# Kernel optimization log

Measured on AMD Instinct MI355X. Metric: run time of the kernel, lower is better.

The kernel has to match this reference:

```python
import jax, jax.numpy as jnp
import numpy as np

N_LAYER, N_HEAD, N_EMBD, D_STATE, VOCAB, N_POS = 12, 12, 768, 128, 60, 1024
ID_ID = 0


def _ln(x, g, b):
    m = x.mean(-1, keepdims=True)
    v = ((x - m) ** 2).mean(-1, keepdims=True)
    return (x - m) / jnp.sqrt(v + 1e-5) * g + b


def _prefix_states(input_ids, mul):
    # POST states: s_0 = id ; s_{t+1} = mul[x_t, s_t] ; states[:, t] = s_{t+1}
    B = input_ids.shape[0]

    def step(s, x_t):
        s2 = mul[x_t, s]
        return s2, s2

    s0 = jnp.full((B,), ID_ID, dtype=input_ids.dtype)
    _, post = jax.lax.scan(step, s0, input_ids.T)  # [T, B]
    return post.T  # [B, T]


def _forward(input_ids, mul, tok_emb, state_emb, state_proj_w, state_proj_b, wpe,
             ln1_g, ln1_b, attn_w, attn_b, attn_proj_w, attn_proj_b,
             ln2_g, ln2_b, fc_w, fc_b, mlp_proj_w, mlp_proj_b,
             lnf_g, lnf_b, head_w, head_b):
    B, T = input_ids.shape
    post = _prefix_states(input_ids, mul)
    # pre_state[t] = s_{t-1}; pre_state[0] = id  (inject_mode='clean')
    pre = jnp.concatenate([jnp.full((B, 1), ID_ID, dtype=post.dtype), post[:, :-1]], axis=1)
    # clean + input_add: mask == 1 at every position, fusion hook inactive
    s = state_emb[pre] @ state_proj_w + state_proj_b  # [B, T, E]
    h = tok_emb[input_ids] + s + wpe[:T]              # GPT-2 adds wpe to inputs_embeds
    causal = jnp.tril(jnp.ones((T, T), dtype=bool))
    scale = 1.0 / np.sqrt(N_EMBD // N_HEAD)
    for l in range(N_LAYER):
        a = _ln(h, ln1_g[l], ln1_b[l])
        q, k, v = jnp.split(a @ attn_w[l] + attn_b[l], 3, axis=-1)
        q = q.reshape(B, T, N_HEAD, -1)
        k = k.reshape(B, T, N_HEAD, -1)
        v = v.reshape(B, T, N_HEAD, -1)
        scores = jnp.einsum('bthd,bshd->bhts', q, k) * scale
        scores = jnp.where(causal, scores, jnp.float32(-1e9))
        p = jax.nn.softmax(scores, axis=-1)
        o = jnp.einsum('bhts,bshd->bthd', p, v).reshape(B, T, N_EMBD)
        h = h + o @ attn_proj_w[l] + attn_proj_b[l]
        m = _ln(h, ln2_g[l], ln2_b[l])
        h = h + jax.nn.gelu(m @ fc_w[l] + fc_b[l], approximate=True) @ mlp_proj_w[l] + mlp_proj_b[l]
    h = _ln(h, lnf_g, lnf_b)
    return h @ head_w + head_b  # logits [B, T, VOCAB]


def setup_inputs():
    key = jax.random.key(0)
    ks = jax.random.split(key, 16)
    B, T = 8, 512
    E, L, DS, V = N_EMBD, N_LAYER, D_STATE, VOCAB
    n = lambda k, shp: jax.random.normal(k, shp, dtype=jnp.float32) * 0.02
    return {
        "input_ids": jax.random.randint(ks[0], (B, T), 0, V),
        "mul": jax.random.randint(ks[1], (V, V), 0, V),
        "tok_emb": n(ks[2], (V, E)),
        "state_emb": n(ks[3], (V, DS)),
        "state_proj_w": n(ks[4], (DS, E)),
        "state_proj_b": jnp.zeros((E,), jnp.float32),
        "wpe": n(ks[5], (N_POS, E)),
        "ln1_g": jnp.ones((L, E), jnp.float32),
        "ln1_b": jnp.zeros((L, E), jnp.float32),
        "attn_w": n(ks[6], (L, E, 3 * E)),
        "attn_b": jnp.zeros((L, 3 * E), jnp.float32),
        "attn_proj_w": n(ks[7], (L, E, E)),
        "attn_proj_b": jnp.zeros((L, E), jnp.float32),
        "ln2_g": jnp.ones((L, E), jnp.float32),
        "ln2_b": jnp.zeros((L, E), jnp.float32),
        "fc_w": n(ks[8], (L, E, 4 * E)),
        "fc_b": jnp.zeros((L, 4 * E), jnp.float32),
        "mlp_proj_w": n(ks[9], (L, 4 * E, E)),
        "mlp_proj_b": jnp.zeros((L, E), jnp.float32),
        "lnf_g": jnp.ones((E,), jnp.float32),
        "lnf_b": jnp.zeros((E,), jnp.float32),
        "head_w": n(ks[10], (E, V)),
        "head_b": jnp.zeros((V,), jnp.float32),
    }


def reference(input_ids, mul, tok_emb, state_emb, state_proj_w, state_proj_b, wpe,
              ln1_g, ln1_b, attn_w, attn_b, attn_proj_w, attn_proj_b,
              ln2_g, ln2_b, fc_w, fc_b, mlp_proj_w, mlp_proj_b,
              lnf_g, lnf_b, head_w, head_b):
    return _forward(input_ids, mul, tok_emb, state_emb, state_proj_w, state_proj_b, wpe,
                    ln1_g, ln1_b, attn_w, attn_b, attn_proj_w, attn_proj_b,
                    ln2_g, ln2_b, fc_w, fc_b, mlp_proj_w, mlp_proj_b,
                    lnf_g, lnf_b, head_w, head_b)
```

## Files before the change

kernel.cpp:

```cpp
#include <hip/hip_runtime.h>
#include <cmath>

using bf16 = __bf16;
typedef __bf16 bf16x8 __attribute__((ext_vector_type(8)));
typedef float f32x4 __attribute__((ext_vector_type(4)));

#define N_LAYER 12
#define EMB 768
#define E3 2304
#define FF 3072
#define SEQ 512
#define NB 8
#define BT 4096
#define NH 12
#define HD 64
#define VOC 60
#define DST 128

__device__ __forceinline__ void gll16(const bf16* g, bf16* l) {
    __builtin_amdgcn_global_load_lds(
        (const __attribute__((address_space(1))) void*)g,
        (__attribute__((address_space(3))) void*)l,
        16, 0, 0);
}

__global__ __launch_bounds__(1024)
void scan_kernel(const int* __restrict__ ids, const int* __restrict__ mul, int* __restrict__ pre)
{
    __shared__ int smul[VOC * VOC];
    __shared__ int sx[SEQ];
    __shared__ int chunk_end[16 * VOC];
    __shared__ int entry[17];
    int b = blockIdx.x;
    int tid = threadIdx.x;
    for (int i = tid; i < VOC * VOC; i += 1024) smul[i] = mul[i];
    for (int i = tid; i < SEQ; i += 1024) sx[i] = ids[b * SEQ + i];
    __syncthreads();
    if (tid < 16 * VOC) {
        int c = tid / VOC, s0 = tid % VOC;
        int s = s0;
        int base = c * 32;
        for (int j = 0; j < 32; j++) s = smul[sx[base + j] * VOC + s];
        chunk_end[c * VOC + s0] = s;
    }
    __syncthreads();
    if (tid == 0) {
        int s = 0;
        entry[0] = 0;
        for (int c = 0; c < 16; c++) { s = chunk_end[c * VOC + s]; entry[c + 1] = s; }
    }
    __syncthreads();
    if (tid < 16) {
        int c = tid;
        int s = entry[c];
        for (int j = 0; j < 32; j++) {
            int t = c * 32 + j;
            pre[b * SEQ + t] = s;
            s = smul[sx[t] * VOC + s];
        }
    }
}

__global__ __launch_bounds__(256)
void pst_kernel(const float* __restrict__ se, const float* __restrict__ w,
                const float* __restrict__ bias, float* __restrict__ pst)
{
    int v = blockIdx.x;
    int e = blockIdx.y * 256 + threadIdx.x;
    float acc = bias[e];
    for (int k = 0; k < DST; k++) acc += se[v * DST + k] * w[k * EMB + e];
    pst[v * EMB + e] = acc;
}

__device__ __forceinline__ void ln_stats(float& s, float& s2, float* ps, int tid)
{
    for (int o = 32; o > 0; o >>= 1) { s += __shfl_xor(s, o, 64); s2 += __shfl_xor(s2, o, 64); }
    int wave = tid >> 6, lane = tid & 63;
    if (lane == 0) { ps[wave] = s; ps[4 + wave] = s2; }
    __syncthreads();
    s = ps[0] + ps[1] + ps[2] + ps[3];
    s2 = ps[4] + ps[5] + ps[6] + ps[7];
}

__global__ __launch_bounds__(256)
void embed_ln_kernel(const int* __restrict__ ids, const int* __restrict__ pre,
                     const float* __restrict__ tok_emb, const float* __restrict__ pst,
                     const float* __restrict__ wpe,
                     const float* __restrict__ g, const float* __restrict__ b,
                     float* __restrict__ h, bf16* __restrict__ y)
{
    int t = blockIdx.x;
    int pos = t & (SEQ - 1);
    int id = ids[t], pr = pre[t];
    int tid = threadIdx.x;
    float vals[3];
    float s = 0.f, s2 = 0.f;
    for (int j = 0; j < 3; j++) {
        int e = tid + j * 256;
        float xv = tok_emb[id * EMB + e] + pst[pr * EMB + e] + wpe[pos * EMB + e];
        h[(size_t)t * EMB + e] = xv;
        vals[j] = xv; s += xv; s2 += xv * xv;
    }
    __shared__ float ps[8];
    ln_stats(s, s2, ps, tid);
    float m = s * (1.0f / EMB);
    float var = s2 * (1.0f / EMB) - m * m;
    float inv = rsqrtf(var + 1e-5f);
    for (int j = 0; j < 3; j++) {
        int e = tid + j * 256;
        y[(size_t)t * EMB + e] = (bf16)((vals[j] - m) * inv * g[e] + b[e]);
    }
}

template<int S>
__global__ __launch_bounds__(256)
void reduce_ln_kernel(const float* __restrict__ p, const float* __restrict__ bias,
                      float* __restrict__ h,
                      const float* __restrict__ g, const float* __restrict__ b,
                      bf16* __restrict__ y)
{
    int t = blockIdx.x;
    int tid = threadIdx.x;
    float vals[3];
    float s = 0.f, s2 = 0.f;
    for (int j = 0; j < 3; j++) {
        int e = tid + j * 256;
        size_t i = (size_t)t * EMB + e;
        float acc = bias[e] + h[i];
        for (int sp = 0; sp < S; sp++) acc += p[(size_t)sp * ((size_t)BT * EMB) + i];
        h[i] = acc;
        vals[j] = acc; s += acc; s2 += acc * acc;
    }
    __shared__ float ps[8];
    ln_stats(s, s2, ps, tid);
    float m = s * (1.0f / EMB);
    float var = s2 * (1.0f / EMB) - m * m;
    float inv = rsqrtf(var + 1e-5f);
    for (int j = 0; j < 3; j++) {
        int e = tid + j * 256;
        y[(size_t)t * EMB + e] = (bf16)((vals[j] - m) * inv * g[e] + b[e]);
    }
}

__global__ __launch_bounds__(256)
void convw_kernel(const float* __restrict__ W, bf16* __restrict__ WT, int K, int N)
{
    __shared__ float tile[32][33];
    int kb = blockIdx.y * 32, nb = blockIdx.x * 32;
    const float* Wl = W + (size_t)blockIdx.z * K * N;
    bf16* WTl = WT + (size_t)blockIdx.z * K * N;
    int tx = threadIdx.x & 31, ty = threadIdx.x >> 5;
    for (int i = ty; i < 32; i += 8) {
        int k = kb + i, n = nb + tx;
        if (k < K && n < N) tile[i][tx] = Wl[(size_t)k * N + n];
    }
    __syncthreads();
    for (int i = ty; i < 32; i += 8) {
        int n = nb + i, k = kb + tx;
        if (k < K && n < N) WTl[(size_t)n * K + k] = (bf16)tile[tx][i];
    }
}

__global__ __launch_bounds__(256)
void vtrans_kernel(const bf16* __restrict__ qkv, bf16* __restrict__ vT)
{
    int bh = blockIdx.y;
    int b = bh / NH, hh = bh - b * NH;
    int idx = blockIdx.x * 256 + threadIdx.x;
    int d = idx >> 9, t = idx & 511;
    vT[((size_t)bh * HD + d) * SEQ + t] = qkv[((size_t)(b * SEQ + t)) * E3 + 2 * EMB + hh * HD + d];
}

__global__ __launch_bounds__(256)
void fattn_kernel(const bf16* __restrict__ qkv, const bf16* __restrict__ vT, bf16* __restrict__ Og)
{
    __shared__ bf16 sK[128 * 64];
    __shared__ bf16 sV[64 * 128];
    __shared__ bf16 sP[4][16 * 128];
    int mq = blockIdx.x;
    int bh = blockIdx.y;
    int b = bh / NH, hh = bh - b * NH;
    int tid = threadIdx.x, lane = tid & 63, wave = tid >> 6;
    int r = lane & 15, q = lane >> 4;

    const bf16* Qg = qkv + (size_t)(b * SEQ + mq * 64) * E3 + hh * HD;
    const bf16* Kg = qkv + (size_t)(b * SEQ) * E3 + EMB + hh * HD;
    const bf16* Vg = vT + (size_t)bh * HD * SEQ;

    bf16x8 af[2];
    {
        const bf16* qrow = Qg + (size_t)(wave * 16 + r) * E3 + q * 8;
        af[0] = *(const bf16x8*)(qrow);
        af[1] = *(const bf16x8*)(qrow + 32);
    }

    float mrun[4], lrun[4];
    f32x4 acco[4];
    for (int e = 0; e < 4; e++) { mrun[e] = -1e30f; lrun[e] = 0.f; }
    for (int no = 0; no < 4; no++)
        for (int e = 0; e < 4; e++) acco[no][e] = 0.f;

    int KT = mq / 2 + 1;
    bf16* sPw = sP[wave];

    for (int kt = 0; kt < KT; kt++) {
        {
            int row = tid >> 3;
            int cb = (tid & 7) * 8;
            for (int rd = 0; rd < 4; rd++) {
                int rr = rd * 32 + row;
                bf16x8 kv = *(const bf16x8*)(Kg + (size_t)(kt * 128 + rr) * E3 + cb);
                *(bf16x8*)(sK + ((rr * 64 + cb) ^ ((rr & 7) << 3))) = kv;
            }
            int rowv = tid >> 4;
            int cbv = (tid & 15) * 8;
            for (int rd = 0; rd < 4; rd++) {
                int rr = rd * 16 + rowv;
                bf16x8 vv = *(const bf16x8*)(Vg + (size_t)rr * SEQ + kt * 128 + cbv);
                *(bf16x8*)(sV + ((rr * 128 + cbv) ^ ((rr & 7) << 3))) = vv;
            }
        }
        __syncthreads();

        f32x4 acc[8];
        for (int ni = 0; ni < 8; ni++)
            for (int e = 0; e < 4; e++) acc[ni][e] = 0.f;
        for (int ks = 0; ks < 2; ks++) {
            for (int ni = 0; ni < 8; ni++) {
                int row = ni * 16 + r;
                bf16x8 bk = *(const bf16x8*)(sK + ((row * 64 + ks * 32 + q * 8) ^ ((row & 7) << 3)));
                acc[ni] = __builtin_amdgcn_mfma_f32_16x16x32_bf16(af[ks], bk, acc[ni], 0, 0, 0);
            }
        }

        bool dm = (kt * 128 + 127) > (mq * 64);
        for (int ni = 0; ni < 8; ni++) {
            int col = kt * 128 + ni * 16 + r;
            for (int e = 0; e < 4; e++) {
                float s = acc[ni][e] * 0.125f;
                if (dm) {
                    int rowg = mq * 64 + wave * 16 + q * 4 + e;
                    if (col > rowg) s = -1e30f;
                }
                acc[ni][e] = s;
            }
        }

        float corr[4];
        for (int e = 0; e < 4; e++) {
            float mx = -1e30f;
            for (int ni = 0; ni < 8; ni++) mx = fmaxf(mx, acc[ni][e]);
            for (int o2 = 1; o2 < 16; o2 <<= 1) mx = fmaxf(mx, __shfl_xor(mx, o2, 64));
            float mn = fmaxf(mrun[e], mx);
            corr[e] = __expf(mrun[e] - mn);
            mrun[e] = mn;
            float ps = 0.f;
            for (int ni = 0; ni < 8; ni++) {
                float p = __expf(acc[ni][e] - mn);
                acc[ni][e] = p;
                ps += p;
            }
            for (int o2 = 1; o2 < 16; o2 <<= 1) ps += __shfl_xor(ps, o2, 64);
            lrun[e] = lrun[e] * corr[e] + ps;
        }
        for (int no = 0; no < 4; no++)
            for (int e = 0; e < 4; e++) acco[no][e] *= corr[e];

        for (int ni = 0; ni < 8; ni++) {
            for (int e = 0; e < 4; e++) {
                int prow = q * 4 + e;
                sPw[(prow * 128 + ni * 16 + r) ^ ((prow & 7) << 3)] = (bf16)acc[ni][e];
            }
        }
        for (int ks2 = 0; ks2 < 4; ks2++) {
            bf16x8 pa = *(const bf16x8*)(sPw + ((r * 128 + ks2 * 32 + q * 8) ^ ((r & 7) << 3)));
            for (int no = 0; no < 4; no++) {
                int row = no * 16 + r;
                bf16x8 bv = *(const bf16x8*)(sV + ((row * 128 + ks2 * 32 + q * 8) ^ ((row & 7) << 3)));
                acco[no] = __builtin_amdgcn_mfma_f32_16x16x32_bf16(pa, bv, acco[no], 0, 0, 0);
            }
        }
        __syncthreads();
    }

    bf16* orow = Og + (size_t)(b * SEQ + mq * 64 + wave * 16) * EMB + hh * HD;
    for (int e = 0; e < 4; e++) {
        float inv = 1.0f / lrun[e];
        for (int no = 0; no < 4; no++)
            orow[(size_t)(q * 4 + e) * EMB + no * 16 + r] = (bf16)(acco[no][e] * inv);
    }
}

__global__ __launch_bounds__(256)
void reduce_head_kernel(const float* __restrict__ p, const float* __restrict__ bias,
                        float* __restrict__ out)
{
    int i = blockIdx.x * 256 + threadIdx.x;
    int c = i % VOC;
    float acc = bias[c];
    for (int s = 0; s < 8; s++) acc += p[(size_t)s * ((size_t)BT * VOC) + i];
    out[i] = acc;
}

template<int MODE, int KSPLIT = 1>
__global__ __launch_bounds__(256)
void gemm_bt(const bf16* __restrict__ Ag, const bf16* __restrict__ Bg,
             const float* __restrict__ bias, bf16* __restrict__ Cb, float* __restrict__ Cf,
             int M, int N, int K, int lda, int ldb, int ldc,
             long long sAb, long long sAh, long long sBb, long long sBh,
             long long sCb, long long sCh)
{
    __shared__ union { bf16 ab[2][128 * 32]; float st[4][16 * 64]; } sm;
    int z = blockIdx.z, zs = 0;
    if constexpr (KSPLIT > 1) { zs = z % KSPLIT; z /= KSPLIT; }
    int zb = z / NH, zh = z - zb * NH;
    Ag += zb * sAb + zh * sAh;
    Bg += zb * sBb + zh * sBh;
    long long coff = zb * sCb + zh * sCh;

    if constexpr (MODE == 6 || MODE == 7) Cf += (size_t)zs * M * ldc;

    int m0 = blockIdx.y * 128, n0 = blockIdx.x * 128;
    int tid = threadIdx.x, lane = tid & 63, wave = tid >> 6;
    int wm = (wave >> 1) * 64, wn = (wave & 1) * 64;
    int r = lane & 15, q = lane >> 4;

    f32x4 acc[4][4];
    for (int mi = 0; mi < 4; mi++)
        for (int ni = 0; ni < 4; ni++)
            for (int e = 0; e < 4; e++) acc[mi][ni][e] = 0.f;

    bf16* la = sm.ab[0];
    bf16* lb = sm.ab[1];
    int srow = wave * 16 + (lane >> 2);
    int scol = (lane & 3) * 8;
    const bf16* pA = Ag + (size_t)(m0 + srow) * lda + scol;
    const bf16* pB = Bg + (size_t)(n0 + srow) * ldb + scol;
    bf16* lA0 = la + (wave * 16) * 32;
    bf16* lA1 = la + (wave * 16 + 64) * 32;
    bf16* lB0 = lb + (wave * 16) * 32;
    bf16* lB1 = lb + (wave * 16 + 64) * 32;
    size_t stepA = (size_t)64 * lda, stepB = (size_t)64 * ldb;

    int kbeg = 0, kend = K;
    if constexpr (KSPLIT > 1) { int Kc = K / KSPLIT; kbeg = zs * Kc; kend = kbeg + Kc; }

    for (int k0 = kbeg; k0 < kend; k0 += 32) {
        gll16(pA + k0, lA0);
        gll16(pA + k0 + stepA, lA1);
        gll16(pB + k0, lB0);
        gll16(pB + k0 + stepB, lB1);
        __syncthreads();
        bf16x8 af[4], bq[4];
        for (int mi = 0; mi < 4; mi++) af[mi] = *(const bf16x8*)(la + (wm + mi * 16 + r) * 32 + q * 8);
        for (int ni = 0; ni < 4; ni++) bq[ni] = *(const bf16x8*)(lb + (wn + ni * 16 + r) * 32 + q * 8);
        for (int mi = 0; mi < 4; mi++)
            for (int ni = 0; ni < 4; ni++)
                acc[mi][ni] = __builtin_amdgcn_mfma_f32_16x16x32_bf16(af[mi], bq[ni], acc[mi][ni], 0, 0, 0);
        __syncthreads();
    }

    if constexpr (MODE == 7) {
        for (int mi = 0; mi < 4; mi++) {
            for (int ni = 0; ni < 4; ni++) {
                int colg = n0 + wn + ni * 16 + r;
                if (colg >= N) continue;
                for (int e = 0; e < 4; e++) {
                    int rowg = m0 + wm + mi * 16 + q * 4 + e;
                    if (rowg >= M) continue;
                    Cf[(size_t)coff + (size_t)rowg * ldc + colg] = acc[mi][ni][e];
                }
            }
        }
        return;
    }

    const float* biasp = (MODE == 6) ? nullptr : bias;

    float* st = sm.st[wave];
    bool wvalid = (n0 + wn) < N;
    for (int mi = 0; mi < 4; mi++) {
        if (wvalid) {
            for (int ni = 0; ni < 4; ni++)
                for (int e = 0; e < 4; e++)
                    st[(q * 4 + e) * 64 + ni * 16 + r] = acc[mi][ni][e];
        }
        asm volatile("s_waitcnt lgkmcnt(0)" ::: "memory");
        if (wvalid) {
            for (int it = 0; it < 2; it++) {
                int task = lane + it * 64;
                int row = task >> 3, cc = (task & 7) * 8;
                f32x4 v0 = *(const f32x4*)(st + row * 64 + cc);
                f32x4 v1 = *(const f32x4*)(st + row * 64 + cc + 4);
                int colg = n0 + wn + cc;
                int rowg = m0 + wm + mi * 16 + row;
                if (biasp) {
                    f32x4 b0 = *(const f32x4*)(biasp + colg);
                    f32x4 b1 = *(const f32x4*)(biasp + colg + 4);
                    v0 += b0; v1 += b1;
                }
                size_t off = (size_t)coff + (size_t)rowg * ldc + colg;
                if constexpr (MODE == 0) {
                    bf16x8 pk;
                    for (int j = 0; j < 4; j++) { pk[j] = (bf16)v0[j]; pk[4 + j] = (bf16)v1[j]; }
                    *(bf16x8*)(Cb + off) = pk;
                } else if constexpr (MODE == 1) {
                    float w[8];
                    for (int j = 0; j < 4; j++) { w[j] = v0[j]; w[4 + j] = v1[j]; }
                    bf16x8 pk;
                    for (int j = 0; j < 8; j++) {
                        float x = w[j];
                        float gx = 0.5f * x * (1.0f + tanhf(0.7978845608028654f * (x + 0.044715f * x * x * x)));
                        pk[j] = (bf16)gx;
                    }
                    *(bf16x8*)(Cb + off) = pk;
                } else {
                    *(f32x4*)(Cf + off) = v0;
                    *(f32x4*)(Cf + off + 4) = v1;
                }
            }
        }
        asm volatile("s_waitcnt lgkmcnt(0)" ::: "memory");
    }
}

extern "C" void kernel_launch(void* const* d_in, const int* in_sizes, int n_in,
                              void* d_out, int out_size, void* d_ws, size_t ws_size,
                              hipStream_t stream)
{
    (void)in_sizes; (void)n_in; (void)out_size; (void)ws_size;
    const int*   input_ids    = (const int*)d_in[0];
    const int*   mul          = (const int*)d_in[1];
    const float* tok_emb      = (const float*)d_in[2];
    const float* state_emb    = (const float*)d_in[3];
    const float* state_proj_w = (const float*)d_in[4];
    const float* state_proj_b = (const float*)d_in[5];
    const float* wpe          = (const float*)d_in[6];
    const float* ln1_g        = (const float*)d_in[7];
    const float* ln1_b        = (const float*)d_in[8];
    const float* attn_w       = (const float*)d_in[9];
    const float* attn_b       = (const float*)d_in[10];
    const float* attn_proj_w  = (const float*)d_in[11];
    const float* attn_proj_b  = (const float*)d_in[12];
    const float* ln2_g        = (const float*)d_in[13];
    const float* ln2_b        = (const float*)d_in[14];
    const float* fc_w         = (const float*)d_in[15];
    const float* fc_b         = (const float*)d_in[16];
    const float* mlp_proj_w   = (const float*)d_in[17];
    const float* mlp_proj_b   = (const float*)d_in[18];
    const float* lnf_g        = (const float*)d_in[19];
    const float* lnf_b        = (const float*)d_in[20];
    const float* head_w       = (const float*)d_in[21];
    const float* head_b       = (const float*)d_in[22];
    float* out = (float*)d_out;

    char* ws = (char*)d_ws;
    size_t off = 0;
    auto alloc = [&](size_t bytes) -> char* {
        char* p = ws + off;
        off += (bytes + 255) & ~(size_t)255;
        return p;
    };
    bf16*  wT_attn = (bf16*)alloc((size_t)N_LAYER * E3 * EMB * 2);
    bf16*  wT_ap   = (bf16*)alloc((size_t)N_LAYER * EMB * EMB * 2);
    bf16*  wT_fc   = (bf16*)alloc((size_t)N_LAYER * FF * EMB * 2);
    bf16*  wT_mp   = (bf16*)alloc((size_t)N_LAYER * EMB * FF * 2);
    bf16*  wT_head = (bf16*)alloc((size_t)VOC * EMB * 2);
    float* pst     = (float*)alloc((size_t)VOC * EMB * 4);
    int*   pre     = (int*)alloc((size_t)BT * 4);
    float* h       = (float*)alloc((size_t)BT * EMB * 4);
    bf16*  xb      = (bf16*)alloc((size_t)BT * EMB * 2);
    bf16*  qkv     = (bf16*)alloc((size_t)BT * E3 * 2);
    bf16*  vT      = (bf16*)alloc((size_t)NB * NH * HD * SEQ * 2);
    bf16*  o       = (bf16*)alloc((size_t)BT * EMB * 2);
    bf16*  fcout   = (bf16*)alloc((size_t)BT * FF * 2);
    float* pbuf    = (float*)alloc((size_t)4 * BT * EMB * 4);

    convw_kernel<<<dim3(E3 / 32, EMB / 32, N_LAYER), 256, 0, stream>>>(attn_w, wT_attn, EMB, E3);
    convw_kernel<<<dim3(EMB / 32, EMB / 32, N_LAYER), 256, 0, stream>>>(attn_proj_w, wT_ap, EMB, EMB);
    convw_kernel<<<dim3(FF / 32, EMB / 32, N_LAYER), 256, 0, stream>>>(fc_w, wT_fc, EMB, FF);
    convw_kernel<<<dim3(EMB / 32, FF / 32, N_LAYER), 256, 0, stream>>>(mlp_proj_w, wT_mp, FF, EMB);
    convw_kernel<<<dim3(2, EMB / 32, 1), 256, 0, stream>>>(head_w, wT_head, EMB, VOC);

    scan_kernel<<<NB, 1024, 0, stream>>>(input_ids, mul, pre);
    pst_kernel<<<dim3(VOC, 3), 256, 0, stream>>>(state_emb, state_proj_w, state_proj_b, pst);
    embed_ln_kernel<<<BT, 256, 0, stream>>>(input_ids, pre, tok_emb, pst, wpe,
                                            ln1_g, ln1_b, h, xb);

    for (int l = 0; l < N_LAYER; l++) {
        gemm_bt<0><<<dim3(E3 / 128, BT / 128, 1), 256, 0, stream>>>(
            xb, wT_attn + (size_t)l * E3 * EMB, attn_b + l * E3, qkv, nullptr,
            BT, E3, EMB, EMB, EMB, E3, 0, 0, 0, 0, 0, 0);
        vtrans_kernel<<<dim3(128, NB * NH), 256, 0, stream>>>(qkv, vT);
        fattn_kernel<<<dim3(SEQ / 64, NB * NH), 256, 0, stream>>>(qkv, vT, o);
        gemm_bt<6, 4><<<dim3(EMB / 128, BT / 128, 4), 256, 0, stream>>>(
            o, wT_ap + (size_t)l * EMB * EMB, nullptr, nullptr, pbuf,
            BT, EMB, EMB, EMB, EMB, EMB, 0, 0, 0, 0, 0, 0);
        reduce_ln_kernel<4><<<BT, 256, 0, stream>>>(
            pbuf, attn_proj_b + l * EMB, h, ln2_g + l * EMB, ln2_b + l * EMB, xb);
        gemm_bt<1><<<dim3(FF / 128, BT / 128, 1), 256, 0, stream>>>(
            xb, wT_fc + (size_t)l * FF * EMB, fc_b + l * FF, fcout, nullptr,
            BT, FF, EMB, EMB, EMB, FF, 0, 0, 0, 0, 0, 0);
        gemm_bt<6, 4><<<dim3(EMB / 128, BT / 128, 4), 256, 0, stream>>>(
            fcout, wT_mp + (size_t)l * EMB * FF, nullptr, nullptr, pbuf,
            BT, EMB, FF, FF, FF, EMB, 0, 0, 0, 0, 0, 0);
        const float* ng = (l < N_LAYER - 1) ? (ln1_g + (l + 1) * EMB) : lnf_g;
        const float* nb2 = (l < N_LAYER - 1) ? (ln1_b + (l + 1) * EMB) : lnf_b;
        reduce_ln_kernel<4><<<BT, 256, 0, stream>>>(
            pbuf, mlp_proj_b + l * EMB, h, ng, nb2, xb);
    }
    gemm_bt<7, 8><<<dim3(1, BT / 128, 8), 256, 0, stream>>>(
        xb, wT_head, nullptr, nullptr, pbuf,
        BT, VOC, EMB, EMB, EMB, VOC, 0, 0, 0, 0, 0, 0);
    reduce_head_kernel<<<(BT * VOC) / 256, 256, 0, stream>>>(pbuf, head_b, out);
}
```

Measured before the change: 2.902 ms.

## Add 256x256 triple-buffered 8-wave GEMM for all transformer layer projections

Introduces a new gemm8 kernel with 512 threads, 256x256 output tiles and a three-stage LDS ring fed by global_load_lds. Each k-step is split into two halves, so loads for the step two ahead overlap the MFMA work, with setprio raised around the MFMA bursts. It replaces the 128x128 double-sync gemm_bt for the QKV, attention projection, FC and MLP projection GEMMs, and trims gemm_bt down to the head-only path. The larger tiles cut A/B refetch and barrier overhead, at the cost of fewer blocks: for example, the split-K projections launch only 3x16x4 = 192 blocks, and the larger LDS footprint limits occupancy.

```diff
diff --git a/kernel.cpp b/kernel.cpp
--- a/kernel.cpp
+++ b/kernel.cpp
@@ -303,22 +303,165 @@
 }
 
 template<int MODE, int KSPLIT = 1>
+__global__ __launch_bounds__(512, 2)
+void gemm8(const bf16* __restrict__ Ag, const bf16* __restrict__ Bg,
+           const float* __restrict__ bias, bf16* __restrict__ Cb, float* __restrict__ Cf,
+           int N, int K, int lda, int ldb, int ldc)
+{
+    __shared__ union {
+        bf16 stage[3][2][256 * 32];
+        float st[8][16 * 64];
+    } sm;
+
+    int zs = blockIdx.z;
+    int Kc = K / KSPLIT;
+    int kbeg = zs * Kc;
+    int NT = Kc / 32;
+    if constexpr (MODE == 6) Cf += (size_t)zs * (size_t)BT * ldc;
+
+    int m0 = blockIdx.y * 256, n0 = blockIdx.x * 256;
+    int tid = threadIdx.x, lane = tid & 63, wave = tid >> 6;
+    int wm = wave >> 2, wn = wave & 3;
+    int r = lane & 15, q = lane >> 4;
+
+    f32x4 acc[8][4];
+#pragma unroll
+    for (int mi = 0; mi < 8; mi++)
+#pragma unroll
+        for (int ni = 0; ni < 4; ni++)
+#pragma unroll
+            for (int e = 0; e < 4; e++) acc[mi][ni][e] = 0.f;
+
+    int srow = lane >> 2;
+    int scol = (lane & 3) * 8;
+    const bf16* pA0 = Ag + (size_t)(m0 + (wave) * 16 + srow) * lda + scol;
+    const bf16* pA1 = Ag + (size_t)(m0 + (8 + wave) * 16 + srow) * lda + scol;
+    const bf16* pB0 = Bg + (size_t)(n0 + (wave) * 16 + srow) * ldb + scol;
+    const bf16* pB1 = Bg + (size_t)(n0 + (8 + wave) * 16 + srow) * ldb + scol;
+    int l0 = wave * 512;
+    int l1 = (8 + wave) * 512;
+
+    auto stageA = [&](int kt, int b) {
+        int k0 = kbeg + kt * 32;
+        gll16(pA0 + k0, &sm.stage[b][0][l0]);
+        gll16(pA1 + k0, &sm.stage[b][0][l1]);
+    };
+    auto stageB = [&](int kt, int b) {
+        int k0 = kbeg + kt * 32;
+        gll16(pB0 + k0, &sm.stage[b][1][l0]);
+        gll16(pB1 + k0, &sm.stage[b][1][l1]);
+    };
+
+    stageA(0, 0); stageB(0, 0);
+    stageA(1 < NT ? 1 : 0, 1); stageB(1 < NT ? 1 : 0, 1);
+    asm volatile("s_waitcnt vmcnt(4)" ::: "memory");
+    __builtin_amdgcn_s_barrier();
+    asm volatile("" ::: "memory");
+
+    for (int t = 0; t < NT; t++) {
+        int c = t % 3;
+        const bf16* la = sm.stage[c][0];
+        const bf16* lb = sm.stage[c][1];
+        int t2 = (t + 2 < NT) ? t + 2 : NT - 1;
+        int b2 = (t + 2) % 3;
+
+        bf16x8 afr[4], bfr[4];
+#pragma unroll
+        for (int i = 0; i < 4; i++)
+            afr[i] = *(const bf16x8*)(la + (wm * 128 + i * 16 + r) * 32 + q * 8);
+#pragma unroll
+        for (int ni = 0; ni < 4; ni++)
+            bfr[ni] = *(const bf16x8*)(lb + (wn * 64 + ni * 16 + r) * 32 + q * 8);
+        stageA(t2, b2);
+        asm volatile("" ::: "memory");
+        __builtin_amdgcn_s_barrier();
+        __builtin_amdgcn_s_setprio(1);
+#pragma unroll
+        for (int i = 0; i < 4; i++)
+#pragma unroll
+            for (int ni = 0; ni < 4; ni++)
+                acc[i][ni] = __builtin_amdgcn_mfma_f32_16x16x32_bf16(afr[i], bfr[ni], acc[i][ni], 0, 0, 0);
+        __builtin_amdgcn_s_setprio(0);
+        asm volatile("" ::: "memory");
+        __builtin_amdgcn_s_barrier();
+        asm volatile("" ::: "memory");
+
+#pragma unroll
+        for (int i = 0; i < 4; i++)
+            afr[i] = *(const bf16x8*)(la + (wm * 128 + (4 + i) * 16 + r) * 32 + q * 8);
+        stageB(t2, b2);
+        asm volatile("" ::: "memory");
+        __builtin_amdgcn_s_barrier();
+        __builtin_amdgcn_s_setprio(1);
+#pragma unroll
+        for (int i = 0; i < 4; i++)
+#pragma unroll
+            for (int ni = 0; ni < 4; ni++)
+                acc[4 + i][ni] = __builtin_amdgcn_mfma_f32_16x16x32_bf16(afr[i], bfr[ni], acc[4 + i][ni], 0, 0, 0);
+        __builtin_amdgcn_s_setprio(0);
+        asm volatile("s_waitcnt vmcnt(4)" ::: "memory");
+        __builtin_amdgcn_s_barrier();
+        asm volatile("" ::: "memory");
+    }
+
+    asm volatile("s_waitcnt vmcnt(0) lgkmcnt(0)" ::: "memory");
+    __builtin_amdgcn_s_barrier();
+    asm volatile("" ::: "memory");
+
+    float* st = sm.st[wave];
+#pragma unroll 1
+    for (int mi = 0; mi < 8; mi++) {
+#pragma unroll
+        for (int ni = 0; ni < 4; ni++)
+#pragma unroll
+            for (int e = 0; e < 4; e++)
+                st[(q * 4 + e) * 64 + ni * 16 + r] = acc[mi][ni][e];
+        asm volatile("s_waitcnt lgkmcnt(0)" ::: "memory");
+        for (int it = 0; it < 2; it++) {
+            int task = lane + it * 64;
+            int row = task >> 3, cc = (task & 7) * 8;
+            f32x4 v0 = *(const f32x4*)(st + row * 64 + cc);
+            f32x4 v1 = *(const f32x4*)(st + row * 64 + cc + 4);
+            int colg = n0 + wn * 64 + cc;
+            int rowg = m0 + wm * 128 + mi * 16 + row;
+            if (MODE != 6 && bias) {
+                f32x4 b0 = *(const f32x4*)(bias + colg);
+                f32x4 b1 = *(const f32x4*)(bias + colg + 4);
+                v0 += b0; v1 += b1;
+            }
+            size_t off = (size_t)rowg * ldc + colg;
+            if constexpr (MODE == 0) {
+                bf16x8 pk;
+                for (int j = 0; j < 4; j++) { pk[j] = (bf16)v0[j]; pk[4 + j] = (bf16)v1[j]; }
+                *(bf16x8*)(Cb + off) = pk;
+            } else if constexpr (MODE == 1) {
+                float w[8];
+                for (int j = 0; j < 4; j++) { w[j] = v0[j]; w[4 + j] = v1[j]; }
+                bf16x8 pk;
+                for (int j = 0; j < 8; j++) {
+                    float x = w[j];
+                    float gx = 0.5f * x * (1.0f + tanhf(0.7978845608028654f * (x + 0.044715f * x * x * x)));
+                    pk[j] = (bf16)gx;
+                }
+                *(bf16x8*)(Cb + off) = pk;
+            } else {
+                *(f32x4*)(Cf + off) = v0;
+                *(f32x4*)(Cf + off + 4) = v1;
+            }
+        }
+        asm volatile("s_waitcnt lgkmcnt(0)" ::: "memory");
+    }
+}
+
+template<int MODE, int KSPLIT = 1>
 __global__ __launch_bounds__(256)
 void gemm_bt(const bf16* __restrict__ Ag, const bf16* __restrict__ Bg,
              const float* __restrict__ bias, bf16* __restrict__ Cb, float* __restrict__ Cf,
-             int M, int N, int K, int lda, int ldb, int ldc,
-             long long sAb, long long sAh, long long sBb, long long sBh,
-             long long sCb, long long sCh)
-{
-    __shared__ union { bf16 ab[2][128 * 32]; float st[4][16 * 64]; } sm;
-    int z = blockIdx.z, zs = 0;
-    if constexpr (KSPLIT > 1) { zs = z % KSPLIT; z /= KSPLIT; }
-    int zb = z / NH, zh = z - zb * NH;
-    Ag += zb * sAb + zh * sAh;
-    Bg += zb * sBb + zh * sBh;
-    long long coff = zb * sCb + zh * sCh;
-
-    if constexpr (MODE == 6 || MODE == 7) Cf += (size_t)zs * M * ldc;
+             int M, int N, int K, int lda, int ldb, int ldc)
+{
+    __shared__ bf16 sab[2][128 * 32];
+    int zs = blockIdx.z % KSPLIT;
+    if constexpr (MODE == 7) Cf += (size_t)zs * M * ldc;
 
     int m0 = blockIdx.y * 128, n0 = blockIdx.x * 128;
     int tid = threadIdx.x, lane = tid & 63, wave = tid >> 6;
@@ -330,8 +473,8 @@
         for (int ni = 0; ni < 4; ni++)
             for (int e = 0; e < 4; e++) acc[mi][ni][e] = 0.f;
 
-    bf16* la = sm.ab[0];
-    bf16* lb = sm.ab[1];
+    bf16* la = sab[0];
+    bf16* lb = sab[1];
     int srow = wave * 16 + (lane >> 2);
     int scol = (lane & 3) * 8;
     const bf16* pA = Ag + (size_t)(m0 + srow) * lda + scol;
@@ -342,8 +485,8 @@
     bf16* lB1 = lb + (wave * 16 + 64) * 32;
     size_t stepA = (size_t)64 * lda, stepB = (size_t)64 * ldb;
 
-    int kbeg = 0, kend = K;
-    if constexpr (KSPLIT > 1) { int Kc = K / KSPLIT; kbeg = zs * Kc; kend = kbeg + Kc; }
+    int Kc = K / KSPLIT;
+    int kbeg = zs * Kc, kend = kbeg + Kc;
 
     for (int k0 = kbeg; k0 < kend; k0 += 32) {
         gll16(pA + k0, lA0);
@@ -360,67 +503,16 @@
         __syncthreads();
     }
 
-    if constexpr (MODE == 7) {
-        for (int mi = 0; mi < 4; mi++) {
-            for (int ni = 0; ni < 4; ni++) {
-                int colg = n0 + wn + ni * 16 + r;
-                if (colg >= N) continue;
-                for (int e = 0; e < 4; e++) {
-                    int rowg = m0 + wm + mi * 16 + q * 4 + e;
-                    if (rowg >= M) continue;
-                    Cf[(size_t)coff + (size_t)rowg * ldc + colg] = acc[mi][ni][e];
-                }
-            }
-        }
-        return;
-    }
-
-    const float* biasp = (MODE == 6) ? nullptr : bias;
-
-    float* st = sm.st[wave];
-    bool wvalid = (n0 + wn) < N;
     for (int mi = 0; mi < 4; mi++) {
-        if (wvalid) {
-            for (int ni = 0; ni < 4; ni++)
-                for (int e = 0; e < 4; e++)
-                    st[(q * 4 + e) * 64 + ni * 16 + r] = acc[mi][ni][e];
-        }
-        asm volatile("s_waitcnt lgkmcnt(0)" ::: "memory");
-        if (wvalid) {
-            for (int it = 0; it < 2; it++) {
-                int task = lane + it * 64;
-                int row = task >> 3, cc = (task & 7) * 8;
-                f32x4 v0 = *(const f32x4*)(st + row * 64 + cc);
-                f32x4 v1 = *(const f32x4*)(st + row * 64 + cc + 4);
-                int colg = n0 + wn + cc;
-                int rowg = m0 + wm + mi * 16 + row;
-                if (biasp) {
-                    f32x4 b0 = *(const f32x4*)(biasp + colg);
-                    f32x4 b1 = *(const f32x4*)(biasp + colg + 4);
-                    v0 += b0; v1 += b1;
-                }
-                size_t off = (size_t)coff + (size_t)rowg * ldc + colg;
-                if constexpr (MODE == 0) {
-                    bf16x8 pk;
-                    for (int j = 0; j < 4; j++) { pk[j] = (bf16)v0[j]; pk[4 + j] = (bf16)v1[j]; }
-                    *(bf16x8*)(Cb + off) = pk;
-                } else if constexpr (MODE == 1) {
-                    float w[8];
-                    for (int j = 0; j < 4; j++) { w[j] = v0[j]; w[4 + j] = v1[j]; }
-                    bf16x8 pk;
-                    for (int j = 0; j < 8; j++) {
-                        float x = w[j];
-                        float gx = 0.5f * x * (1.0f + tanhf(0.7978845608028654f * (x + 0.044715f * x * x * x)));
-                        pk[j] = (bf16)gx;
-                    }
-                    *(bf16x8*)(Cb + off) = pk;
-                } else {
-                    *(f32x4*)(Cf + off) = v0;
-                    *(f32x4*)(Cf + off + 4) = v1;
-                }
-            }
-        }
-        asm volatile("s_waitcnt lgkmcnt(0)" ::: "memory");
+        for (int ni = 0; ni < 4; ni++) {
+            int colg = n0 + wn + ni * 16 + r;
+            if (colg >= N) continue;
+            for (int e = 0; e < 4; e++) {
+                int rowg = m0 + wm + mi * 16 + q * 4 + e;
+                if (rowg >= M) continue;
+                Cf[(size_t)rowg * ldc + colg] = acc[mi][ni][e];
+            }
+        }
     }
 }
 
@@ -488,22 +580,22 @@
                                             ln1_g, ln1_b, h, xb);
 
     for (int l = 0; l < N_LAYER; l++) {
-        gemm_bt<0><<<dim3(E3 / 128, BT / 128, 1), 256, 0, stream>>>(
+        gemm8<0><<<dim3(E3 / 256, BT / 256, 1), 512, 0, stream>>>(
             xb, wT_attn + (size_t)l * E3 * EMB, attn_b + l * E3, qkv, nullptr,
-            BT, E3, EMB, EMB, EMB, E3, 0, 0, 0, 0, 0, 0);
+            E3, EMB, EMB, EMB, E3);
         vtrans_kernel<<<dim3(128, NB * NH), 256, 0, stream>>>(qkv, vT);
         fattn_kernel<<<dim3(SEQ / 64, NB * NH), 256, 0, stream>>>(qkv, vT, o);
-        gemm_bt<6, 4><<<dim3(EMB / 128, BT / 128, 4), 256, 0, stream>>>(
+        gemm8<6, 4><<<dim3(EMB / 256, BT / 256, 4), 512, 0, stream>>>(
             o, wT_ap + (size_t)l * EMB * EMB, nullptr, nullptr, pbuf,
-            BT, EMB, EMB, EMB, EMB, EMB, 0, 0, 0, 0, 0, 0);
+            EMB, EMB, EMB, EMB, EMB);
         reduce_ln_kernel<4><<<BT, 256, 0, stream>>>(
             pbuf, attn_proj_b + l * EMB, h, ln2_g + l * EMB, ln2_b + l * EMB, xb);
-        gemm_bt<1><<<dim3(FF / 128, BT / 128, 1), 256, 0, stream>>>(
+        gemm8<1><<<dim3(FF / 256, BT / 256, 1), 512, 0, stream>>>(
             xb, wT_fc + (size_t)l * FF * EMB, fc_b + l * FF, fcout, nullptr,
-            BT, FF, EMB, EMB, EMB, FF, 0, 0, 0, 0, 0, 0);
-        gemm_bt<6, 4><<<dim3(EMB / 128, BT / 128, 4), 256, 0, stream>>>(
+            FF, EMB, EMB, EMB, FF);
+        gemm8<6, 4><<<dim3(EMB / 256, BT / 256, 4), 512, 0, stream>>>(
             fcout, wT_mp + (size_t)l * EMB * FF, nullptr, nullptr, pbuf,
-            BT, EMB, FF, FF, FF, EMB, 0, 0, 0, 0, 0, 0);
+            EMB, FF, FF, FF, EMB);
         const float* ng = (l < N_LAYER - 1) ? (ln1_g + (l + 1) * EMB) : lnf_g;
         const float* nb2 = (l < N_LAYER - 1) ? (ln1_b + (l + 1) * EMB) : lnf_b;
         reduce_ln_kernel<4><<<BT, 256, 0, stream>>>(
@@ -511,6 +603,6 @@
     }
     gemm_bt<7, 8><<<dim3(1, BT / 128, 8), 256, 0, stream>>>(
         xb, wT_head, nullptr, nullptr, pbuf,
-        BT, VOC, EMB, EMB, EMB, VOC, 0, 0, 0, 0, 0, 0);
+        BT, VOC, EMB, EMB, EMB, VOC);
     reduce_head_kernel<<<(BT * VOC) / 256, 256, 0, stream>>>(pbuf, head_b, out);
 }
```

Result: slower. 3.987 ms (+37.4%).

## Fuse V transpose into QKV GEMM epilogue and add XCD block remapping

Applied to the files above, without the earlier changes.

The QKV GEMM epilogue now also writes the V columns in transposed per-head layout, which removes the separate vtrans kernel launch and its extra read of qkv. A block-index swizzle spreads neighbouring tiles across XCDs for the GEMM and attention kernels to improve L2 locality. The epilogue staging buffer stride is padded to 68 floats to reduce LDS bank conflicts. The cost is that V is stored with strided 2-byte scalar writes, which coalesce poorly.

```diff
diff --git a/kernel.cpp b/kernel.cpp
--- a/kernel.cpp
+++ b/kernel.cpp
@@ -22,6 +22,18 @@
         (const __attribute__((address_space(1))) void*)g,
         (__attribute__((address_space(3))) void*)l,
         16, 0, 0);
+}
+
+__device__ __forceinline__ void xcd_remap(int& bx, int& by, int& bz)
+{
+    int gx = gridDim.x, gy = gridDim.y, gz = gridDim.z;
+    int nwg = gx * gy * gz;
+    int lin = (blockIdx.z * gy + blockIdx.y) * gx + blockIdx.x;
+    int swz = (lin & 7) * (nwg >> 3) + (lin >> 3);
+    bx = swz % gx;
+    int t = swz / gx;
+    by = t % gy;
+    bz = t / gy;
 }
 
 __global__ __launch_bounds__(1024)
@@ -162,23 +174,13 @@
 }
 
 __global__ __launch_bounds__(256)
-void vtrans_kernel(const bf16* __restrict__ qkv, bf16* __restrict__ vT)
-{
-    int bh = blockIdx.y;
-    int b = bh / NH, hh = bh - b * NH;
-    int idx = blockIdx.x * 256 + threadIdx.x;
-    int d = idx >> 9, t = idx & 511;
-    vT[((size_t)bh * HD + d) * SEQ + t] = qkv[((size_t)(b * SEQ + t)) * E3 + 2 * EMB + hh * HD + d];
-}
-
-__global__ __launch_bounds__(256)
 void fattn_kernel(const bf16* __restrict__ qkv, const bf16* __restrict__ vT, bf16* __restrict__ Og)
 {
     __shared__ bf16 sK[128 * 64];
     __shared__ bf16 sV[64 * 128];
     __shared__ bf16 sP[4][16 * 128];
-    int mq = blockIdx.x;
-    int bh = blockIdx.y;
+    int mq, bh, bzu;
+    xcd_remap(mq, bh, bzu);
     int b = bh / NH, hh = bh - b * NH;
     int tid = threadIdx.x, lane = tid & 63, wave = tid >> 6;
     int r = lane & 15, q = lane >> 4;
@@ -306,21 +308,16 @@
 __global__ __launch_bounds__(256)
 void gemm_bt(const bf16* __restrict__ Ag, const bf16* __restrict__ Bg,
              const float* __restrict__ bias, bf16* __restrict__ Cb, float* __restrict__ Cf,
-             int M, int N, int K, int lda, int ldb, int ldc,
-             long long sAb, long long sAh, long long sBb, long long sBh,
-             long long sCb, long long sCh)
-{
-    __shared__ union { bf16 ab[2][128 * 32]; float st[4][16 * 64]; } sm;
-    int z = blockIdx.z, zs = 0;
-    if constexpr (KSPLIT > 1) { zs = z % KSPLIT; z /= KSPLIT; }
-    int zb = z / NH, zh = z - zb * NH;
-    Ag += zb * sAb + zh * sAh;
-    Bg += zb * sBb + zh * sBh;
-    long long coff = zb * sCb + zh * sCh;
-
+             bf16* __restrict__ Vt,
+             int M, int N, int K, int lda, int ldb, int ldc)
+{
+    __shared__ union { bf16 ab[2][128 * 32]; float st[4][16 * 68]; } sm;
+    int bx, by, bz;
+    xcd_remap(bx, by, bz);
+    int zs = bz;
     if constexpr (MODE == 6 || MODE == 7) Cf += (size_t)zs * M * ldc;
 
-    int m0 = blockIdx.y * 128, n0 = blockIdx.x * 128;
+    int m0 = by * 128, n0 = bx * 128;
     int tid = threadIdx.x, lane = tid & 63, wave = tid >> 6;
     int wm = (wave >> 1) * 64, wn = (wave & 1) * 64;
     int r = lane & 15, q = lane >> 4;
@@ -342,8 +339,8 @@
     bf16* lB1 = lb + (wave * 16 + 64) * 32;
     size_t stepA = (size_t)64 * lda, stepB = (size_t)64 * ldb;
 
-    int kbeg = 0, kend = K;
-    if constexpr (KSPLIT > 1) { int Kc = K / KSPLIT; kbeg = zs * Kc; kend = kbeg + Kc; }
+    int Kc = K / KSPLIT;
+    int kbeg = zs * Kc, kend = kbeg + Kc;
 
     for (int k0 = kbeg; k0 < kend; k0 += 32) {
         gll16(pA + k0, lA0);
@@ -368,7 +365,7 @@
                 for (int e = 0; e < 4; e++) {
                     int rowg = m0 + wm + mi * 16 + q * 4 + e;
                     if (rowg >= M) continue;
-                    Cf[(size_t)coff + (size_t)rowg * ldc + colg] = acc[mi][ni][e];
+                    Cf[(size_t)rowg * ldc + colg] = acc[mi][ni][e];
                 }
             }
         }
@@ -378,46 +375,49 @@
     const float* biasp = (MODE == 6) ? nullptr : bias;
 
     float* st = sm.st[wave];
-    bool wvalid = (n0 + wn) < N;
     for (int mi = 0; mi < 4; mi++) {
-        if (wvalid) {
-            for (int ni = 0; ni < 4; ni++)
-                for (int e = 0; e < 4; e++)
-                    st[(q * 4 + e) * 64 + ni * 16 + r] = acc[mi][ni][e];
-        }
+        for (int ni = 0; ni < 4; ni++)
+            for (int e = 0; e < 4; e++)
+                st[(q * 4 + e) * 68 + ni * 16 + r] = acc[mi][ni][e];
         asm volatile("s_waitcnt lgkmcnt(0)" ::: "memory");
-        if (wvalid) {
-            for (int it = 0; it < 2; it++) {
-                int task = lane + it * 64;
-                int row = task >> 3, cc = (task & 7) * 8;
-                f32x4 v0 = *(const f32x4*)(st + row * 64 + cc);
-                f32x4 v1 = *(const f32x4*)(st + row * 64 + cc + 4);
-                int colg = n0 + wn + cc;
-                int rowg = m0 + wm + mi * 16 + row;
-                if (biasp) {
-                    f32x4 b0 = *(const f32x4*)(biasp + colg);
-                    f32x4 b1 = *(const f32x4*)(biasp + colg + 4);
-                    v0 += b0; v1 += b1;
+        for (int it = 0; it < 2; it++) {
+            int task = lane + it * 64;
+            int row = task >> 3, cc = (task & 7) * 8;
+            f32x4 v0 = *(const f32x4*)(st + row * 68 + cc);
+            f32x4 v1 = *(const f32x4*)(st + row * 68 + cc + 4);
+            int colg = n0 + wn + cc;
+            int rowg = m0 + wm + mi * 16 + row;
+            if (biasp) {
+                f32x4 b0 = *(const f32x4*)(biasp + colg);
+                f32x4 b1 = *(const f32x4*)(biasp + colg + 4);
+                v0 += b0; v1 += b1;
+            }
+            size_t off = (size_t)rowg * ldc + colg;
+            if constexpr (MODE == 8) {
+                bf16x8 pk;
+                for (int j = 0; j < 4; j++) { pk[j] = (bf16)v0[j]; pk[4 + j] = (bf16)v1[j]; }
+                *(bf16x8*)(Cb + off) = pk;
+                if (colg >= 2 * EMB) {
+                    int hh = (colg - 2 * EMB) >> 6;
+                    int d0 = (colg - 2 * EMB) & 63;
+                    int bb = rowg >> 9, tt = rowg & 511;
+                    bf16* vp = Vt + (((size_t)(bb * NH + hh) * HD + d0) * SEQ + tt);
+#pragma unroll
+                    for (int j = 0; j < 8; j++) vp[(size_t)j * SEQ] = pk[j];
                 }
-                size_t off = (size_t)coff + (size_t)rowg * ldc + colg;
-                if constexpr (MODE == 0) {
-                    bf16x8 pk;
-                    for (int j = 0; j < 4; j++) { pk[j] = (bf16)v0[j]; pk[4 + j] = (bf16)v1[j]; }
-                    *(bf16x8*)(Cb + off) = pk;
-                } else if constexpr (MODE == 1) {
-                    float w[8];
-                    for (int j = 0; j < 4; j++) { w[j] = v0[j]; w[4 + j] = v1[j]; }
-                    bf16x8 pk;
-                    for (int j = 0; j < 8; j++) {
-                        float x = w[j];
-                        float gx = 0.5f * x * (1.0f + tanhf(0.7978845608028654f * (x + 0.044715f * x * x * x)));
-                        pk[j] = (bf16)gx;
-                    }
-                    *(bf16x8*)(Cb + off) = pk;
-                } else {
-                    *(f32x4*)(Cf + off) = v0;
-                    *(f32x4*)(Cf + off + 4) = v1;
+            } else if constexpr (MODE == 1) {
+                float w[8];
+                for (int j = 0; j < 4; j++) { w[j] = v0[j]; w[4 + j] = v1[j]; }
+                bf16x8 pk;
+                for (int j = 0; j < 8; j++) {
+                    float x = w[j];
+                    float gx = 0.5f * x * (1.0f + tanhf(0.7978845608028654f * (x + 0.044715f * x * x * x)));
+                    pk[j] = (bf16)gx;
                 }
+                *(bf16x8*)(Cb + off) = pk;
+            } else {
+                *(f32x4*)(Cf + off) = v0;
+                *(f32x4*)(Cf + off + 4) = v1;
             }
         }
         asm volatile("s_waitcnt lgkmcnt(0)" ::: "memory");
@@ -488,29 +488,28 @@
                                             ln1_g, ln1_b, h, xb);
 
     for (int l = 0; l < N_LAYER; l++) {
-        gemm_bt<0><<<dim3(E3 / 128, BT / 128, 1), 256, 0, stream>>>(
-            xb, wT_attn + (size_t)l * E3 * EMB, attn_b + l * E3, qkv, nullptr,
-            BT, E3, EMB, EMB, EMB, E3, 0, 0, 0, 0, 0, 0);
-        vtrans_kernel<<<dim3(128, NB * NH), 256, 0, stream>>>(qkv, vT);
+        gemm_bt<8><<<dim3(E3 / 128, BT / 128, 1), 256, 0, stream>>>(
+            xb, wT_attn + (size_t)l * E3 * EMB, attn_b + l * E3, qkv, nullptr, vT,
+            BT, E3, EMB, EMB, EMB, E3);
         fattn_kernel<<<dim3(SEQ / 64, NB * NH), 256, 0, stream>>>(qkv, vT, o);
         gemm_bt<6, 4><<<dim3(EMB / 128, BT / 128, 4), 256, 0, stream>>>(
-            o, wT_ap + (size_t)l * EMB * EMB, nullptr, nullptr, pbuf,
-            BT, EMB, EMB, EMB, EMB, EMB, 0, 0, 0, 0, 0, 0);
+            o, wT_ap + (size_t)l * EMB * EMB, nullptr, nullptr, pbuf, nullptr,
+            BT, EMB, EMB, EMB, EMB, EMB);
         reduce_ln_kernel<4><<<BT, 256, 0, stream>>>(
             pbuf, attn_proj_b + l * EMB, h, ln2_g + l * EMB, ln2_b + l * EMB, xb);
         gemm_bt<1><<<dim3(FF / 128, BT / 128, 1), 256, 0, stream>>>(
-            xb, wT_fc + (size_t)l * FF * EMB, fc_b + l * FF, fcout, nullptr,
-            BT, FF, EMB, EMB, EMB, FF, 0, 0, 0, 0, 0, 0);
+            xb, wT_fc + (size_t)l * FF * EMB, fc_b + l * FF, fcout, nullptr, nullptr,
+            BT, FF, EMB, EMB, EMB, FF);
         gemm_bt<6, 4><<<dim3(EMB / 128, BT / 128, 4), 256, 0, stream>>>(
-            fcout, wT_mp + (size_t)l * EMB * FF, nullptr, nullptr, pbuf,
-            BT, EMB, FF, FF, FF, EMB, 0, 0, 0, 0, 0, 0);
+            fcout, wT_mp + (size_t)l * EMB * FF, nullptr, nullptr, pbuf, nullptr,
+            BT, EMB, FF, FF, FF, EMB);
         const float* ng = (l < N_LAYER - 1) ? (ln1_g + (l + 1) * EMB) : lnf_g;
         const float* nb2 = (l < N_LAYER - 1) ? (ln1_b + (l + 1) * EMB) : lnf_b;
         reduce_ln_kernel<4><<<BT, 256, 0, stream>>>(
             pbuf, mlp_proj_b + l * EMB, h, ng, nb2, xb);
     }
     gemm_bt<7, 8><<<dim3(1, BT / 128, 8), 256, 0, stream>>>(
-        xb, wT_head, nullptr, nullptr, pbuf,
-        BT, VOC, EMB, EMB, EMB, VOC, 0, 0, 0, 0, 0, 0);
+        xb, wT_head, nullptr, nullptr, pbuf, nullptr,
+        BT, VOC, EMB, EMB, EMB, VOC);
     reduce_head_kernel<<<(BT * VOC) / 256, 256, 0, stream>>>(pbuf, head_b, out);
 }
```

New measurement: 2.652 ms. 8.6% less time.
